# Kernel tuning notes

Hardware: AMD Instinct MI355X
Metric: run time of the kernel (lower is better)

Reference implementation:

```python
import jax, jax.numpy as jnp
import numpy as np

D_MODEL = 2048
N_HEADS = 32
N_KVHEADS = 8
HEAD_DIM = D_MODEL // N_HEADS  # 64
N_GROUPS = N_HEADS // N_KVHEADS  # 4
B, L = 2, 2048


def setup_inputs() -> dict:
    key = jax.random.key(0)
    k1, k2, k3 = jax.random.split(key, 3)
    x = jax.random.normal(k1, (B, L, D_MODEL), dtype=jnp.float32)
    W_qkv = jax.random.normal(k2, (D_MODEL, HEAD_DIM * (N_HEADS + 2 * N_KVHEADS)), dtype=jnp.float32) * 0.02
    W_out = jax.random.normal(k3, (D_MODEL, D_MODEL), dtype=jnp.float32) * 0.02
    # additive causal mask, broadcasts over (b, g, h, l, j)
    neg = jnp.float32(-1e9)
    mask = jnp.where(jnp.tril(jnp.ones((L, L), dtype=bool)), jnp.float32(0.0), neg)
    return {"x": x, "mask": mask, "W_qkv": W_qkv, "W_out": W_out}


def reference(x, mask, W_qkv, W_out):
    b, l, _ = x.shape
    qkv = x @ W_qkv  # (b, l, hd*(H + 2*KVH))
    q, k, v = jnp.split(qkv, [N_HEADS * HEAD_DIM, (N_HEADS + N_KVHEADS) * HEAD_DIM], axis=-1)
    # NOTE: faithful to the original: plain row-major reshapes (no seq/head transpose)
    q = q.reshape(b, N_GROUPS, N_KVHEADS, l, HEAD_DIM)  # (b, g, h, l, d)
    k = k.reshape(b, N_KVHEADS, l, HEAD_DIM)            # (b, h, j, d)
    v = v.reshape(b, N_KVHEADS, l, HEAD_DIM)            # (b, h, j, d)
    scores = jnp.einsum('bghld,bhjd->bghlj', q, k) * (HEAD_DIM ** -0.5)
    scores = scores + mask  # mask broadcasts over leading dims
    attn = jax.nn.softmax(scores, axis=-1)
    out = jnp.einsum('bghlj,bhjd->bghld', attn, v)  # (b, g, h, l, d)
    # rearrange 'b g h l d -> b l (g h d)'
    out = jnp.transpose(out, (0, 3, 1, 2, 4)).reshape(b, l, D_MODEL)
    return out @ W_out
```

## Files before the change

### kernel.cpp

```cpp
#include <hip/hip_runtime.h>
#include <stdint.h>


typedef unsigned short u16;
typedef unsigned int u32;
typedef __attribute__((ext_vector_type(8))) short bf16x8;
typedef __attribute__((ext_vector_type(4))) float f32x4;

__device__ __forceinline__ u16 f2bf(float f) {
  union { float f; uint32_t u; } v; v.f = f;
  uint32_t u = v.u;
  u += 0x7fffu + ((u >> 16) & 1u);
  return (u16)(u >> 16);
}

__device__ __forceinline__ f32x4 mfma16(bf16x8 a, bf16x8 b, f32x4 c) {
  return __builtin_amdgcn_mfma_f32_16x16x32_bf16(a, b, c, 0, 0, 0);
}

__device__ __forceinline__ uint32_t cvt_pk_bf16(float a, float b) {
  uint32_t r;
  asm("v_cvt_pk_bf16_f32 %0, %1, %2" : "=v"(r) : "v"(a), "v"(b));
  return r;
}

__device__ __forceinline__ float exp2fast(float x) {
  return __builtin_amdgcn_exp2f(x);
}

__device__ __forceinline__ void gload16(const u16* g, u16* l) {
  __builtin_amdgcn_global_load_lds((__attribute__((address_space(1))) void*)g,
                                   (__attribute__((address_space(3))) void*)l, 16, 0, 0);
}

__global__ __launch_bounds__(256) void cvt_f32_bf16(const float* __restrict__ in,
                                                    u16* __restrict__ out, int n4) {
  int i = blockIdx.x * blockDim.x + threadIdx.x;
  if (i < n4) {
    float4 v = ((const float4*)in)[i];
    uint2 o;
    o.x = (uint32_t)f2bf(v.x) | ((uint32_t)f2bf(v.y) << 16);
    o.y = (uint32_t)f2bf(v.z) | ((uint32_t)f2bf(v.w) << 16);
    ((uint2*)out)[i] = o;
  }
}

__global__ __launch_bounds__(256) void transpose_cvt(const float* __restrict__ in,
                                                     u16* __restrict__ out, int R, int C) {
  __shared__ float tile[32][33];
  int c0 = blockIdx.x * 32, r0 = blockIdx.y * 32;
  int tx = threadIdx.x, ty = threadIdx.y;
#pragma unroll
  for (int k = 0; k < 32; k += 8)
    tile[ty + k][tx] = in[(size_t)(r0 + ty + k) * C + c0 + tx];
  __syncthreads();
#pragma unroll
  for (int k = 0; k < 32; k += 8)
    out[(size_t)(c0 + ty + k) * R + r0 + tx] = f2bf(tile[tx][ty + k]);
}

template <bool OUTF32>
__global__ __launch_bounds__(256) void gemm_bf16(const u16* __restrict__ A,
                                                 const u16* __restrict__ Bt,
                                                 void* __restrict__ C,
                                                 int M, int N, int K) {
  __shared__ __align__(16) u16 As[3][128 * 32];
  __shared__ __align__(16) u16 Bs[3][128 * 32];
  int tid = threadIdx.x;
  int lane = tid & 63, w = tid >> 6;
  int wm = (w >> 1) * 64, wn = (w & 1) * 64;

  int nwg = gridDim.x * gridDim.y;
  int lin = blockIdx.y * gridDim.x + blockIdx.x;
  int lin2 = (lin & 7) * (nwg >> 3) + (lin >> 3);
  int bxs = lin2 % gridDim.x, bys = lin2 / gridDim.x;
  int bm = bys * 128, bn = bxs * 128;

  int c = lane & 15, g = lane >> 4;

  const int srow = w * 16 + (lane >> 2);
  const int scol = (((lane & 3) ^ ((lane >> 3) & 3))) * 8;
  const u16* aP = A + (size_t)(bm + srow) * K + scol;
  const u16* bP = Bt + (size_t)(bn + srow) * K + scol;
  const size_t rowskip = (size_t)64 * K;

  f32x4 zero = {0.f, 0.f, 0.f, 0.f};
  f32x4 acc[4][4];
#pragma unroll
  for (int mi = 0; mi < 4; mi++)
#pragma unroll
    for (int ni = 0; ni < 4; ni++) acc[mi][ni] = zero;

  auto STAGE = [&](int kt, int buf) {
    u16* aL = &As[buf][(w * 16) * 32];
    u16* bL = &Bs[buf][(w * 16) * 32];
    gload16(aP + kt, aL);
    gload16(aP + kt + rowskip, aL + 64 * 32);
    gload16(bP + kt, bL);
    gload16(bP + kt + rowskip, bL + 64 * 32);
  };

  const int nk = K >> 5;
  STAGE(0, 0);
  STAGE(32, 1);
  asm volatile("s_waitcnt vmcnt(0)" ::: "memory");
  __builtin_amdgcn_s_barrier();

  const int fq = (g ^ ((c >> 1) & 3)) * 8;

  for (int t = 0; t < nk; ++t) {
    const int cur = t % 3;
    if (t + 2 < nk) {
      STAGE((t + 2) << 5, (t + 2) % 3);
      asm volatile("s_waitcnt vmcnt(8)" ::: "memory");
    } else if (t + 1 < nk) {
      asm volatile("s_waitcnt vmcnt(4)" ::: "memory");
    } else {
      asm volatile("s_waitcnt vmcnt(0)" ::: "memory");
    }
    __builtin_amdgcn_s_barrier();
    asm volatile("" ::: "memory");
    bf16x8 af[4], bfr[4];
#pragma unroll
    for (int i = 0; i < 4; i++) af[i] = *(const bf16x8*)&As[cur][(wm + i * 16 + c) * 32 + fq];
#pragma unroll
    for (int i = 0; i < 4; i++) bfr[i] = *(const bf16x8*)&Bs[cur][(wn + i * 16 + c) * 32 + fq];
#pragma unroll
    for (int mi = 0; mi < 4; mi++)
#pragma unroll
      for (int ni = 0; ni < 4; ni++)
        acc[mi][ni] = mfma16(af[mi], bfr[ni], acc[mi][ni]);
    asm volatile("" ::: "memory");
    __builtin_amdgcn_s_barrier();
  }

#pragma unroll
  for (int mi = 0; mi < 4; mi++)
#pragma unroll
    for (int ni = 0; ni < 4; ni++)
#pragma unroll
      for (int i = 0; i < 4; i++) {
        int row = bm + wm + mi * 16 + g * 4 + i;
        int col = bn + wn + ni * 16 + c;
        float v = acc[mi][ni][i];
        if (OUTF32)
          ((float*)C)[(size_t)row * N + col] = v;
        else
          ((u16*)C)[(size_t)row * N + col] = f2bf(v);
      }
}

__global__ __launch_bounds__(256, 2) void attn_fwd(const u16* __restrict__ qkv,
                                                   u16* __restrict__ attn) {
  __shared__ __align__(16) u16 Ks[2][64][72];
  __shared__ __align__(16) u16 Vs[2][64][72];
  __shared__ __align__(16) u16 Ps[4][32][64];
  const int tid = threadIdx.x;
  const int lane = tid & 63, w = tid >> 6;
  const int c = lane & 15, g = lane >> 4;
  const float C2 = 0.18033688011112042f;

  const int bid = blockIdx.x;
  const int slot = bid >> 3;
  const int head = (bid & 7) * 8 + (slot >> 3);
  const int p = slot & 7;
  const int qtA = p, qtB = 15 - p;
  const int b = head >> 5, gh = head & 31, h = gh & 7;
  const u16* qb = qkv + (size_t)b * 6291456;
  const int qbaseA = qtA * 128 + w * 32;
  const int qbaseB = qtB * 128 + w * 32;

  const u16* qrowA = qb + (size_t)(gh * 64 + qtA * 4 + w) * 3072;
  const u16* qrowB = qb + (size_t)(gh * 64 + qtB * 4 + w) * 3072;
  bf16x8 qfA[2][2], qfB[2][2];
#pragma unroll
  for (int qs = 0; qs < 2; qs++)
#pragma unroll
    for (int kd = 0; kd < 2; kd++) {
      qfA[qs][kd] = *(const bf16x8*)(qrowA + (qs * 16 + c) * 64 + kd * 32 + g * 8);
      qfB[qs][kd] = *(const bf16x8*)(qrowB + (qs * 16 + c) * 64 + kd * 32 + g * 8);
    }

  const f32x4 zero = {0.f, 0.f, 0.f, 0.f};
  f32x4 oA[2][4], oB[2][4];
#pragma unroll
  for (int qs = 0; qs < 2; qs++)
#pragma unroll
    for (int dt = 0; dt < 4; dt++) { oA[qs][dt] = zero; oB[qs][dt] = zero; }
  float sA[2] = {0.f, 0.f};
  float sB[2] = {0.f, 0.f};

  const int kj = tid >> 2, kd16 = (tid & 3) * 16;
  const int vj0 = (tid >> 4) * 4, vd = (tid & 15) * 4;
  const int vsw = (tid & 7) << 3;
  uint4 kreg0, kreg1;
  uint2 vreg[4];

  auto LOAD = [&](int t) {
    int j = t * 64 + kj;
    const u16* kr = qb + (size_t)(h * 256 + (j >> 3)) * 3072 + 2048 + (j & 7) * 64;
    kreg0 = *(const uint4*)(kr + kd16);
    kreg1 = *(const uint4*)(kr + kd16 + 8);
#pragma unroll
    for (int r = 0; r < 4; r++) {
      int jv = t * 64 + vj0 + r;
      const u16* vr = qb + (size_t)(h * 256 + (jv >> 3)) * 3072 + 2560 + (jv & 7) * 64;
      vreg[r] = *(const uint2*)(vr + vd);
    }
  };
  auto EX = [](uint2 v, int e) -> uint32_t {
    uint32_t x = (e < 2) ? v.x : v.y;
    return (e & 1) ? (x >> 16) : (x & 0xffffu);
  };
  auto STORE = [&](int buf) {
    *(uint4*)&Ks[buf][kj][kd16] = kreg0;
    *(uint4*)&Ks[buf][kj][kd16 + 8] = kreg1;
#pragma unroll
    for (int e = 0; e < 4; e++) {
      uint2 wv;
      wv.x = EX(vreg[0], e) | (EX(vreg[1], e) << 16);
      wv.y = EX(vreg[2], e) | (EX(vreg[3], e) << 16);
      *(uint2*)&Vs[buf][vd + e][vj0 ^ vsw] = wv;
    }
  };

  auto computeQ = [&](int t, int qbase, bf16x8 (&qf)[2][2], bf16x8 (&kf)[4][2],
                      f32x4 (&o)[2][4], float (&s_i)[2], int cur) {
    const bool diag = (t * 64 + 63 > qbase);
#pragma unroll
    for (int qs = 0; qs < 2; qs++) {
      f32x4 sc[4];
      __builtin_amdgcn_s_setprio(1);
#pragma unroll
      for (int kvt = 0; kvt < 4; kvt++) {
        f32x4 s = mfma16(kf[kvt][0], qf[qs][0], zero);
        sc[kvt] = mfma16(kf[kvt][1], qf[qs][1], s);
      }
      __builtin_amdgcn_s_setprio(0);
      const int q = qbase + qs * 16 + c;
      if (diag) {
#pragma unroll
        for (int kvt = 0; kvt < 4; kvt++)
#pragma unroll
          for (int i = 0; i < 4; i++)
            if (t * 64 + kvt * 16 + g * 4 + i > q) sc[kvt][i] = -1e30f;
      }
      float rs = 0.f;
#pragma unroll
      for (int kvt = 0; kvt < 4; kvt++)
#pragma unroll
        for (int i = 0; i < 4; i++) {
          float pv = exp2fast(sc[kvt][i] * C2);
          sc[kvt][i] = pv;
          rs += pv;
        }
      rs += __shfl_xor(rs, 16);
      rs += __shfl_xor(rs, 32);
      s_i[qs] += rs;
      const int pr = qs * 16 + c;
      const int sw = (c & 7) << 3;
#pragma unroll
      for (int kvt = 0; kvt < 4; kvt++) {
        uint2 pw;
        pw.x = cvt_pk_bf16(sc[kvt][0], sc[kvt][1]);
        pw.y = cvt_pk_bf16(sc[kvt][2], sc[kvt][3]);
        *(uint2*)&Ps[w][pr][(kvt * 16 + g * 4) ^ sw] = pw;
      }
    }
    __builtin_amdgcn_s_setprio(1);
#pragma unroll
    for (int kt2 = 0; kt2 < 2; kt2++) {
      bf16x8 bv[4];
#pragma unroll
      for (int dt = 0; dt < 4; dt++) {
        const int vr = dt * 16 + c;
        const int sv = ((dt * 4 + (c >> 2)) & 7) << 3;
        bv[dt] = *(const bf16x8*)&Vs[cur][vr][(kt2 * 32 + g * 8) ^ sv];
      }
#pragma unroll
      for (int qs = 0; qs < 2; qs++) {
        const int pr = qs * 16 + c;
        bf16x8 pa = *(const bf16x8*)&Ps[w][pr][(kt2 * 32 + g * 8) ^ ((c & 7) << 3)];
#pragma unroll
        for (int dt = 0; dt < 4; dt++) o[qs][dt] = mfma16(pa, bv[dt], o[qs][dt]);
      }
    }
    __builtin_amdgcn_s_setprio(0);
  };

  const int nt = 2 * qtB + 2;
  const int jtA = (qbaseA + 31) >> 6;
  const int jtB = (qbaseB + 31) >> 6;

  LOAD(0);
  STORE(0);
  __syncthreads();

  for (int t = 0; t < nt; ++t) {
    const int cur = t & 1;
    if (t + 1 < nt) LOAD(t + 1);
    if (t <= jtB) {
      bf16x8 kf[4][2];
#pragma unroll
      for (int kvt = 0; kvt < 4; kvt++)
#pragma unroll
        for (int kd = 0; kd < 2; kd++)
          kf[kvt][kd] = *(const bf16x8*)&Ks[cur][kvt * 16 + c][kd * 32 + g * 8];
      if (t <= jtA) computeQ(t, qbaseA, qfA, kf, oA, sA, cur);
      computeQ(t, qbaseB, qfB, kf, oB, sB, cur);
    }
    if (t + 1 < nt) STORE(cur ^ 1);
    __syncthreads();
  }

  auto epi = [&](int qbase, f32x4 (&o)[2][4], float (&s_i)[2]) {
#pragma unroll
    for (int qs = 0; qs < 2; qs++)
#pragma unroll
      for (int i = 0; i < 4; i++) {
        float sd = __shfl(s_i[qs], g * 4 + i);
        float inv = 1.0f / sd;
        int row = qbase + qs * 16 + g * 4 + i;
        u16* orow = attn + ((size_t)(b * 2048 + row)) * 2048 + gh * 64;
#pragma unroll
        for (int dt = 0; dt < 4; dt++) orow[dt * 16 + c] = f2bf(o[qs][dt][i] * inv);
      }
  };
  epi(qbaseA, oA, sA);
  epi(qbaseB, oB, sB);
}

extern "C" void kernel_launch(void* const* d_in, const int* in_sizes, int n_in,
                              void* d_out, int out_size, void* d_ws, size_t ws_size,
                              hipStream_t stream) {
  const float* x = (const float*)d_in[0];
  const float* Wqkv = (const float*)d_in[2];
  const float* Wout = (const float*)d_in[3];
  float* out = (float*)d_out;

  u16* xb = (u16*)d_ws;
  u16* wqkvT = xb + 8388608;
  u16* woutT = wqkvT + 6291456;
  u16* qkv = woutT + 4194304;
  u16* attn = qkv + 12582912;

  cvt_f32_bf16<<<8192, 256, 0, stream>>>(x, xb, 2097152);
  transpose_cvt<<<dim3(3072 / 32, 2048 / 32), dim3(32, 8), 0, stream>>>(Wqkv, wqkvT, 2048, 3072);
  transpose_cvt<<<dim3(2048 / 32, 2048 / 32), dim3(32, 8), 0, stream>>>(Wout, woutT, 2048, 2048);
  gemm_bf16<false><<<dim3(3072 / 128, 4096 / 128), 256, 0, stream>>>(xb, wqkvT, qkv, 4096, 3072, 2048);
  attn_fwd<<<512, 256, 0, stream>>>(qkv, attn);
  gemm_bf16<true><<<dim3(2048 / 128, 4096 / 128), 256, 0, stream>>>(attn, woutT, out, 4096, 2048, 2048);
}
```

Measured before the change: 189.7 us.

## Single-buffer K/V shared tiles and raise attention occupancy to four blocks

```diff
diff --git a/kernel.cpp b/kernel.cpp
--- a/kernel.cpp
+++ b/kernel.cpp
@@ -150,10 +150,10 @@
       }
 }
 
-__global__ __launch_bounds__(256, 2) void attn_fwd(const u16* __restrict__ qkv,
+__global__ __launch_bounds__(256, 4) void attn_fwd(const u16* __restrict__ qkv,
                                                    u16* __restrict__ attn) {
-  __shared__ __align__(16) u16 Ks[2][64][72];
-  __shared__ __align__(16) u16 Vs[2][64][72];
+  __shared__ __align__(16) u16 Ks[64][72];
+  __shared__ __align__(16) u16 Vs[64][72];
   __shared__ __align__(16) u16 Ps[4][32][64];
   const int tid = threadIdx.x;
   const int lane = tid & 63, w = tid >> 6;
@@ -212,20 +212,20 @@
     uint32_t x = (e < 2) ? v.x : v.y;
     return (e & 1) ? (x >> 16) : (x & 0xffffu);
   };
-  auto STORE = [&](int buf) {
-    *(uint4*)&Ks[buf][kj][kd16] = kreg0;
-    *(uint4*)&Ks[buf][kj][kd16 + 8] = kreg1;
+  auto STORE = [&]() {
+    *(uint4*)&Ks[kj][kd16] = kreg0;
+    *(uint4*)&Ks[kj][kd16 + 8] = kreg1;
 #pragma unroll
     for (int e = 0; e < 4; e++) {
       uint2 wv;
       wv.x = EX(vreg[0], e) | (EX(vreg[1], e) << 16);
       wv.y = EX(vreg[2], e) | (EX(vreg[3], e) << 16);
-      *(uint2*)&Vs[buf][vd + e][vj0 ^ vsw] = wv;
+      *(uint2*)&Vs[vd + e][vj0 ^ vsw] = wv;
     }
   };
 
   auto computeQ = [&](int t, int qbase, bf16x8 (&qf)[2][2], bf16x8 (&kf)[4][2],
-                      f32x4 (&o)[2][4], float (&s_i)[2], int cur) {
+                      f32x4 (&o)[2][4], float (&s_i)[2]) {
     const bool diag = (t * 64 + 63 > qbase);
 #pragma unroll
     for (int qs = 0; qs < 2; qs++) {
@@ -275,7 +275,7 @@
       for (int dt = 0; dt < 4; dt++) {
         const int vr = dt * 16 + c;
         const int sv = ((dt * 4 + (c >> 2)) & 7) << 3;
-        bv[dt] = *(const bf16x8*)&Vs[cur][vr][(kt2 * 32 + g * 8) ^ sv];
+        bv[dt] = *(const bf16x8*)&Vs[vr][(kt2 * 32 + g * 8) ^ sv];
       }
 #pragma unroll
       for (int qs = 0; qs < 2; qs++) {
@@ -293,11 +293,10 @@
   const int jtB = (qbaseB + 31) >> 6;
 
   LOAD(0);
-  STORE(0);
+  STORE();
   __syncthreads();
 
   for (int t = 0; t < nt; ++t) {
-    const int cur = t & 1;
     if (t + 1 < nt) LOAD(t + 1);
     if (t <= jtB) {
       bf16x8 kf[4][2];
@@ -305,12 +304,15 @@
       for (int kvt = 0; kvt < 4; kvt++)
 #pragma unroll
         for (int kd = 0; kd < 2; kd++)
-          kf[kvt][kd] = *(const bf16x8*)&Ks[cur][kvt * 16 + c][kd * 32 + g * 8];
-      if (t <= jtA) computeQ(t, qbaseA, qfA, kf, oA, sA, cur);
-      computeQ(t, qbaseB, qfB, kf, oB, sB, cur);
-    }
-    if (t + 1 < nt) STORE(cur ^ 1);
-    __syncthreads();
+          kf[kvt][kd] = *(const bf16x8*)&Ks[kvt * 16 + c][kd * 32 + g * 8];
+      if (t <= jtA) computeQ(t, qbaseA, qfA, kf, oA, sA);
+      computeQ(t, qbaseB, qfB, kf, oB, sB);
+    }
+    if (t + 1 < nt) {
+      __syncthreads();
+      STORE();
+      __syncthreads();
+    }
   }
 
   auto epi = [&](int qbase, f32x4 (&o)[2][4], float (&s_i)[2]) {
```

After: 393.8 us. 108% more time.
